# Kernel tuning notes

Hardware: AMD Instinct MI355X
Metric: run time of the kernel (lower is better)

Reference implementation:

```python
import jax, jax.numpy as jnp
import numpy as np

B, S, E, H = 1, 2048, 2048, 16
D = E // H  # head_dim = 128
EPS = 1e-6
NEG_INF = -1e30


def _rms_norm(x, gamma):
    # RMSNorm over last dim: x / sqrt(mean(x^2)+eps) * gamma
    return x * jax.lax.rsqrt(jnp.mean(x * x, axis=-1, keepdims=True) + EPS) * gamma


def _rotate_half(x):
    x1, x2 = jnp.split(x, 2, axis=-1)
    return jnp.concatenate([-x2, x1], axis=-1)


def _rope(x, cos, sin):
    # x: [B,H,S,D]; cos/sin: [S,D] broadcast over batch and heads
    return x * cos + _rotate_half(x) * sin


def setup_inputs() -> dict:
    key = jax.random.key(0)
    ks = jax.random.split(key, 5)
    sc = lambda n: 1.0 / np.sqrt(n)
    x = jax.random.normal(ks[0], (B, S, E), jnp.float32)
    # realistic RoPE tables
    inv_freq = 1.0 / (10000.0 ** (jnp.arange(0, D, 2, dtype=jnp.float32) / D))
    t = jnp.arange(S, dtype=jnp.float32)
    freqs = jnp.outer(t, inv_freq)                    # [S, D/2]
    emb = jnp.concatenate([freqs, freqs], axis=-1)    # [S, D]
    cos, sin = jnp.cos(emb), jnp.sin(emb)
    Wq = jax.random.normal(ks[1], (E, E), jnp.float32) * sc(E)
    Wk = jax.random.normal(ks[2], (D, E), jnp.float32) * sc(E)
    Wv = jax.random.normal(ks[3], (D, E), jnp.float32) * sc(E)
    Wo = jax.random.normal(ks[4], (E, E), jnp.float32) * sc(E)
    q_gamma = jnp.ones((D,), jnp.float32)
    k_gamma = jnp.ones((D,), jnp.float32)
    return dict(x=x, cos=cos, sin=sin, Wq=Wq, Wk=Wk, Wv=Wv, Wo=Wo,
                q_gamma=q_gamma, k_gamma=k_gamma)


def reference(x, cos, sin, Wq, Wk, Wv, Wo, q_gamma, k_gamma):
    # projections (Linear with bias=False -> x @ W.T)
    Q = (x @ Wq.T).reshape(B, S, H, D).transpose(0, 2, 1, 3)  # [B,H,S,D]
    K = (x @ Wk.T)[:, None, :, :]                             # [B,1,S,D]
    V = x @ Wv.T                                              # [B,S,D] (single KV head)
    # qk-norm
    Q = _rms_norm(Q, q_gamma)
    K = _rms_norm(K, k_gamma)  # computed then discarded below (faithful to source)
    # RoPE — source bug replicated: K is overwritten with roped Q
    Q = _rope(Q, cos, sin)
    K = _rope(Q, cos, sin)     # [B,H,S,D]
    # causal attention (dense stand-in for flash_attn_func, scale 1/sqrt(D))
    scores = jnp.einsum('bhqd,bhkd->bhqk', Q, K) / jnp.sqrt(jnp.float32(D))
    causal = jnp.tril(jnp.ones((S, S), bool))
    scores = jnp.where(causal, scores, NEG_INF)
    probs = jax.nn.softmax(scores, axis=-1)
    # single V head broadcast across query heads
    out = jnp.einsum('bhqk,bkd->bqhd', probs, V).reshape(B, S, E)
    return out @ Wo.T
```

## Files before the change

kernel.cpp:

```cpp
#include <hip/hip_runtime.h>
#include <hip/hip_bf16.h>

#define SL 2048
#define NH 16
#define HD 128
#define EMB 2048

typedef __attribute__((ext_vector_type(8))) __bf16 bf16x8;
typedef __attribute__((ext_vector_type(4))) float f32x4;
typedef __attribute__((ext_vector_type(8))) short short8;

__device__ __forceinline__ short bf16bits(float x) {
  union { __hip_bfloat16 h; short s; } u;
  u.h = __float2bfloat16(x);
  return u.s;
}

__device__ __forceinline__ float fexp2(float x) {
  return __builtin_amdgcn_exp2f(x);
}

#define GLDS16(gp, lp) __builtin_amdgcn_global_load_lds( \
    (__attribute__((address_space(1))) void*)(gp), \
    (__attribute__((address_space(3))) void*)(lp), 16, 0, 0)

__global__ __launch_bounds__(256) void cast_all(const float* __restrict__ x,
                                                const float* __restrict__ Wq,
                                                const float* __restrict__ Wv,
                                                const float* __restrict__ Wo,
                                                short* __restrict__ xb,
                                                short* __restrict__ wqvb,
                                                short* __restrict__ wob) {
  long i = ((long)blockIdx.x * 256 + threadIdx.x) * 8;
  const float* in; short* out; long off;
  if (i < 4194304)      { in = x;  out = xb;             off = i; }
  else if (i < 8388608) { in = Wq; out = wqvb;           off = i - 4194304; }
  else if (i < 8650752) { in = Wv; out = wqvb + 4194304; off = i - 8388608; }
  else                  { in = Wo; out = wob;            off = i - 8650752; }
  float4 a = *(const float4*)(in + off);
  float4 b = *(const float4*)(in + off + 4);
  short8 o;
  o[0] = bf16bits(a.x); o[1] = bf16bits(a.y); o[2] = bf16bits(a.z); o[3] = bf16bits(a.w);
  o[4] = bf16bits(b.x); o[5] = bf16bits(b.y); o[6] = bf16bits(b.z); o[7] = bf16bits(b.w);
  *(short8*)(out + off) = o;
}

template<int MODE>
__global__ __launch_bounds__(1024, 1) void gemm128(const short* __restrict__ A,
                                                   const short* __restrict__ B,
                                                   float* __restrict__ C,
                                                   short* __restrict__ Qb,
                                                   short* __restrict__ Kb,
                                                   const float* __restrict__ cosT,
                                                   const float* __restrict__ sinT,
                                                   const float* __restrict__ gamma) {
  __shared__ char arena[131072];
  short* As = (short*)arena;
  const int K = 2048;
  int id = blockIdx.x;
  int nid = (id & 7) * 32 + (id >> 3);
  int tn = nid >> 4, tm = nid & 15;
  int tid = threadIdx.x;
  int w = tid >> 6, lane = tid & 63;
  int g = lane >> 4, c = lane & 15;
  int wr = w >> 2, wc = w & 3;
  const short* Ab = A + (long)(tm * 128) * K;
  const short* Bb = B + (long)(tn * 128) * K;
  int lr = lane >> 3;
  int lsw = (lane & 7) ^ lr;
  int wS = w & 7;
  const short* Sb = (w < 8) ? Ab : Bb;
  int soff = (w < 8) ? 0 : 8192;
  f32x4 zero = {0.f, 0.f, 0.f, 0.f};
  f32x4 acc[2][2];
#pragma unroll
  for (int m = 0; m < 2; ++m)
#pragma unroll
    for (int n = 0; n < 2; ++n) acc[m][n] = zero;

#define STG(buf, kt) do { \
    _Pragma("unroll") \
    for (int j = 0; j < 2; ++j) { \
      int grp = wS * 2 + j; \
      GLDS16(Sb + (long)(grp * 8 + lr) * K + (kt) + lsw * 8, \
             As + (buf) * 16384 + soff + grp * 512); \
    } } while (0)

  STG(0, 0);
  STG(1, 64);
  STG(2, 128);
  asm volatile("s_waitcnt vmcnt(4)" ::: "memory");
  __builtin_amdgcn_s_barrier();

  for (int it = 0; it < 32; ++it) {
    int bf = it & 3;
    if (it < 29) STG((it + 3) & 3, (it + 3) * 64);
    const short* Ax = As + bf * 16384;
    const short* Bx = Ax + 8192;
    bf16x8 af[2][2], bfr[2][2];
#pragma unroll
    for (int kk = 0; kk < 2; ++kk) {
      int ch = ((kk * 4 + g) ^ (c & 7)) * 8;
#pragma unroll
      for (int m = 0; m < 2; ++m)
        af[kk][m] = *(const bf16x8*)(Ax + (wr * 32 + m * 16 + c) * 64 + ch);
#pragma unroll
      for (int n = 0; n < 2; ++n)
        bfr[kk][n] = *(const bf16x8*)(Bx + (wc * 32 + n * 16 + c) * 64 + ch);
    }
    __builtin_amdgcn_s_setprio(1);
#pragma unroll
    for (int kk = 0; kk < 2; ++kk)
#pragma unroll
      for (int m = 0; m < 2; ++m)
#pragma unroll
        for (int n = 0; n < 2; ++n)
          acc[m][n] = __builtin_amdgcn_mfma_f32_16x16x32_bf16(af[kk][m], bfr[kk][n],
                                                              acc[m][n], 0, 0, 0);
    __builtin_amdgcn_s_setprio(0);
    if (it < 29) {
      asm volatile("s_waitcnt vmcnt(4)" ::: "memory");
    } else if (it == 29) {
      asm volatile("s_waitcnt vmcnt(2)" ::: "memory");
    } else if (it == 30) {
      asm volatile("s_waitcnt vmcnt(0)" ::: "memory");
    }
    if (it < 31) __builtin_amdgcn_s_barrier();
  }
#undef STG

  if constexpr (MODE == 0) {
#pragma unroll
    for (int m = 0; m < 2; ++m)
#pragma unroll
      for (int n = 0; n < 2; ++n)
#pragma unroll
        for (int r = 0; r < 4; ++r) {
          int row = tm * 128 + wr * 32 + m * 16 + g * 4 + r;
          int col = tn * 128 + wc * 32 + n * 16 + c;
          C[(long)row * 2048 + col] = acc[m][n][r];
        }
  } else {
    float* xch = (float*)arena;
    float* ssb = (float*)(arena + 65536);
    float ssmr[2][4];
#pragma unroll
    for (int m = 0; m < 2; ++m)
#pragma unroll
      for (int r = 0; r < 4; ++r) {
        float s = acc[m][0][r] * acc[m][0][r] + acc[m][1][r] * acc[m][1][r];
#pragma unroll
        for (int off = 1; off <= 8; off <<= 1) s += __shfl_xor(s, off, 64);
        ssmr[m][r] = s;
      }
    if (c == 0) {
#pragma unroll
      for (int m = 0; m < 2; ++m)
#pragma unroll
        for (int r = 0; r < 4; ++r)
          ssb[wc * 128 + wr * 32 + m * 16 + g * 4 + r] = ssmr[m][r];
    }
#pragma unroll
    for (int m = 0; m < 2; ++m)
#pragma unroll
      for (int n = 0; n < 2; ++n)
#pragma unroll
        for (int r = 0; r < 4; ++r)
          xch[(wr * 32 + m * 16 + g * 4 + r) * 128 + wc * 32 + n * 16 + c] = acc[m][n][r];
    __syncthreads();
    float rn[2][4];
#pragma unroll
    for (int m = 0; m < 2; ++m)
#pragma unroll
      for (int r = 0; r < 4; ++r) {
        int rl = wr * 32 + m * 16 + g * 4 + r;
        float s4 = ssb[rl] + ssb[128 + rl] + ssb[256 + rl] + ssb[384 + rl];
        rn[m][r] = rsqrtf(s4 * (1.0f / 128.0f) + 1e-6f);
      }
    float sgn = (wc < 2) ? -1.f : 1.f;
    float g_own[2], g_par[2];
#pragma unroll
    for (int n = 0; n < 2; ++n) {
      int d = wc * 32 + n * 16 + c;
      g_own[n] = gamma[d];
      g_par[n] = gamma[d ^ 64];
    }
    const float QSC = 0.08838834764831845f * 1.4426950408889634f;
#pragma unroll
    for (int m = 0; m < 2; ++m)
#pragma unroll
      for (int n = 0; n < 2; ++n)
#pragma unroll
        for (int r = 0; r < 4; ++r) {
          int rl = wr * 32 + m * 16 + g * 4 + r;
          int s = tm * 128 + rl;
          int d = wc * 32 + n * 16 + c;
          int u = (wc & 1) * 32 + n * 16 + c;
          float cv = cosT[s * 128 + u];
          float sv = sinT[s * 128 + u];
          float xo = acc[m][n][r] * rn[m][r] * g_own[n];
          float xq = xch[rl * 128 + (d ^ 64)] * rn[m][r] * g_par[n];
          float y  = xo * cv + sgn * xq * sv;
          float yp = xq * cv - sgn * xo * sv;
          float kk = y * cv + sgn * yp * sv;
          long o = ((long)tn * SL + s) * HD + d;
          Qb[o] = bf16bits(y * QSC);
          Kb[o] = bf16bits(kk);
        }
  }
}

__global__ __launch_bounds__(256, 3) void gemm64v(const short* __restrict__ A,
                                                  const short* __restrict__ B,
                                                  short* __restrict__ VT) {
  __shared__ char lds_raw[36864];
  short* As = (short*)lds_raw;
  short* Bs = (short*)(lds_raw + 12288);
  const int K = 2048;
  int nwg = gridDim.x;
  int id = blockIdx.x;
  int nid = (id & 7) * (nwg >> 3) + (id >> 3);
  int tn = 16;
  int tm = nid & 31;
  int tid = threadIdx.x;
  int wave = tid >> 6, lane = tid & 63;
  int g = lane >> 4, c = lane & 15;
  int wr = wave >> 1, wc = wave & 1;
  const short* Ab = A + (long)(tm * 64) * K;
  const short* Bb = B + (long)(tn * 128) * K;
  int swz = (lane & 3) ^ ((lane >> 3) & 3);
  int rdc = (g ^ ((c >> 1) & 3)) * 8;
  f32x4 zero = {0.f, 0.f, 0.f, 0.f};
  f32x4 acc[2][4];
#pragma unroll
  for (int m = 0; m < 2; ++m)
#pragma unroll
    for (int n = 0; n < 4; ++n) acc[m][n] = zero;

#define STG(buf, kt) do { \
    GLDS16(Ab + (long)(wave * 16 + (lane >> 2)) * K + (kt) + swz * 8, \
           As + (buf) * 2048 + wave * 512); \
    _Pragma("unroll") \
    for (int hh = 0; hh < 2; ++hh) { \
      int rb = wave * 32 + hh * 16; \
      GLDS16(Bb + (long)(rb + (lane >> 2)) * K + (kt) + swz * 8, \
             Bs + (buf) * 4096 + rb * 32); \
    } } while (0)

  STG(0, 0);
  STG(1, 32);
  asm volatile("s_waitcnt vmcnt(3)" ::: "memory");
  __builtin_amdgcn_s_barrier();

  int b0 = 0, b1 = 1, b2 = 2;
  for (int it = 0; it < 64; ++it) {
    if (it < 62) STG(b2, (it + 2) * 32);
    bf16x8 a[2], b[4];
#pragma unroll
    for (int m = 0; m < 2; ++m)
      a[m] = *(const bf16x8*)(As + b0 * 2048 + (wr * 32 + m * 16 + c) * 32 + rdc);
#pragma unroll
    for (int n = 0; n < 4; ++n)
      b[n] = *(const bf16x8*)(Bs + b0 * 4096 + (wc * 64 + n * 16 + c) * 32 + rdc);
    __builtin_amdgcn_s_setprio(1);
#pragma unroll
    for (int m = 0; m < 2; ++m)
#pragma unroll
      for (int n = 0; n < 4; ++n)
        acc[m][n] = __builtin_amdgcn_mfma_f32_16x16x32_bf16(a[m], b[n], acc[m][n], 0, 0, 0);
    __builtin_amdgcn_s_setprio(0);
    if (it < 62) {
      asm volatile("s_waitcnt vmcnt(3)" ::: "memory");
      __builtin_amdgcn_s_barrier();
    } else if (it == 62) {
      asm volatile("s_waitcnt vmcnt(0)" ::: "memory");
      __builtin_amdgcn_s_barrier();
    }
    int t = b0; b0 = b1; b1 = b2; b2 = t;
  }
#undef STG

#pragma unroll
  for (int m = 0; m < 2; ++m)
#pragma unroll
    for (int n = 0; n < 4; ++n)
#pragma unroll
      for (int r = 0; r < 4; ++r) {
        int s = tm * 64 + wr * 32 + m * 16 + g * 4 + r;
        int d = wc * 64 + n * 16 + c;
        VT[(long)d * SL + s] = bf16bits(acc[m][n][r]);
      }
}

__global__ __launch_bounds__(256, 2) void attn_part(const short* __restrict__ Qb,
                                                    const short* __restrict__ Kb,
                                                    const short* __restrict__ VTg,
                                                    short* __restrict__ att,
                                                    float* __restrict__ pO,
                                                    float* __restrict__ pml) {
  __shared__ short Ks[2][64 * 128];
  __shared__ short Vs[2][128 * 64];
  __shared__ short Ps[4][16 * 72];
  int wave = threadIdx.x >> 6, lane = threadIdx.x & 63;
  int g = lane >> 4, c = lane & 15;
  int id = blockIdx.x;
  int h = ((id & 7) << 1) | (id >> 8);
  int x = (id >> 3) & 15;
  int cbk = (id >> 7) & 1;
  const short* Qh = Qb + (long)h * SL * HD;
  const short* Kh = Kb + (long)h * SL * HD;
  f32x4 zero = {0.f, 0.f, 0.f, 0.f};
  const float THR2 = 11.541560327111707f;

  int pqt[2], plo[2], pcnt[2], pout[2];
  if (cbk == 0) {
    pqt[0] = x;      plo[0] = 0;      pcnt[0] = x + 1;  pout[0] = 0;
    pqt[1] = 31 - x; plo[1] = 0;      pcnt[1] = 16 - x; pout[1] = 1;
  } else {
    pqt[0] = 31 - x; plo[0] = 16 - x; pcnt[0] = 16;     pout[0] = 2;
    pqt[1] = 0;      plo[1] = 0;      pcnt[1] = 0;      pout[1] = 0;
  }
  int total = pcnt[0] + pcnt[1];

#define ASTAGE(b, kvb) do { \
    _Pragma("unroll") \
    for (int i = 0; i < 4; ++i) { \
      int rb = wave * 16 + i * 4; \
      int row = rb + (lane >> 4); \
      int c16 = (lane & 15) ^ (row & 7); \
      GLDS16(Kh + (long)((kvb) + row) * HD + c16 * 8, &Ks[b][rb * 128]); \
    } \
    _Pragma("unroll") \
    for (int i = 0; i < 4; ++i) { \
      int dbase = i * 32 + wave * 8; \
      int drow = dbase + (lane >> 3); \
      int u8 = (lane & 7) ^ (drow & 7); \
      GLDS16(VTg + (long)drow * SL + (kvb) + u8 * 8, &Vs[b][dbase * 64]); \
    } } while (0)

  ASTAGE(0, plo[0] * 64);
  int s = 0;

  for (int p = 0; p < 2; ++p) {
    int nt = pcnt[p];
    if (nt == 0) break;
    int qt = pqt[p];
    int qb = qt * 64 + wave * 16;
    int qown = qb + c;

    bf16x8 aq[4];
#pragma unroll
    for (int kc = 0; kc < 4; ++kc)
      aq[kc] = *(const bf16x8*)(Qh + (long)qown * HD + kc * 32 + g * 8);

    float m = -1e30f, l = 0.f;
    f32x4 O[8];
#pragma unroll
    for (int d8 = 0; d8 < 8; ++d8) O[d8] = zero;

    for (int i = 0; i < nt; ++i, ++s) {
      int kt = plo[p] + i;
      int kvb = kt * 64;
      int bcu = s & 1;
      asm volatile("s_waitcnt vmcnt(0)" ::: "memory");
      __builtin_amdgcn_s_barrier();
      {
        int ns = s + 1;
        if (ns < total) {
          int np = (ns < pcnt[0]) ? 0 : 1;
          int nkt = plo[np] + (ns - (np ? pcnt[0] : 0));
          ASTAGE(bcu ^ 1, nkt * 64);
        }
      }

      f32x4 sf[4];
#pragma unroll
      for (int n = 0; n < 4; ++n) sf[n] = zero;
      __builtin_amdgcn_s_setprio(1);
#pragma unroll
      for (int kc = 0; kc < 4; ++kc)
#pragma unroll
        for (int n = 0; n < 4; ++n) {
          int row = n * 16 + c;
          int u = (kc * 4 + g) ^ (row & 7);
          bf16x8 bk = *(const bf16x8*)(&Ks[bcu][row * 128 + u * 8]);
          sf[n] = __builtin_amdgcn_mfma_f32_16x16x32_bf16(bk, aq[kc], sf[n], 0, 0, 0);
        }
      __builtin_amdgcn_s_setprio(0);

      float pm = -1e30f;
      if (kt == qt) {
#pragma unroll
        for (int n = 0; n < 4; ++n) {
#pragma unroll
          for (int r = 0; r < 4; ++r) {
            int k = kvb + n * 16 + g * 4 + r;
            if (k > qown) sf[n][r] = -1e30f;
          }
          float a0 = fmaxf(sf[n][0], sf[n][1]);
          float a1 = fmaxf(sf[n][2], sf[n][3]);
          pm = fmaxf(pm, fmaxf(a0, a1));
        }
      } else {
#pragma unroll
        for (int n = 0; n < 4; ++n) {
          float a0 = fmaxf(sf[n][0], sf[n][1]);
          float a1 = fmaxf(sf[n][2], sf[n][3]);
          pm = fmaxf(pm, fmaxf(a0, a1));
        }
      }
      pm = fmaxf(pm, __shfl_xor(pm, 16, 64));
      pm = fmaxf(pm, __shfl_xor(pm, 32, 64));

      if (__any(pm > m + THR2)) {
        float mn_ = fmaxf(m, pm);
        float corr = fexp2(m - mn_);
        m = mn_;
        l *= corr;
        float c4[4];
#pragma unroll
        for (int r = 0; r < 4; ++r) c4[r] = __shfl(corr, g * 4 + r, 64);
#pragma unroll
        for (int d8 = 0; d8 < 8; ++d8)
#pragma unroll
          for (int r = 0; r < 4; ++r) O[d8][r] *= c4[r];
      }

#pragma unroll
      for (int n = 0; n < 4; ++n) {
        float p0 = fexp2(sf[n][0] - m);
        float p1 = fexp2(sf[n][1] - m);
        float p2 = fexp2(sf[n][2] - m);
        float p3 = fexp2(sf[n][3] - m);
        l += (p0 + p1) + (p2 + p3);
        unsigned lo = (unsigned)(unsigned short)bf16bits(p0) |
                      ((unsigned)(unsigned short)bf16bits(p1) << 16);
        unsigned hi = (unsigned)(unsigned short)bf16bits(p2) |
                      ((unsigned)(unsigned short)bf16bits(p3) << 16);
        unsigned long long pq = (unsigned long long)lo | ((unsigned long long)hi << 32);
        *(unsigned long long*)&Ps[wave][c * 72 + n * 16 + g * 4] = pq;
      }

#pragma unroll
      for (int k2 = 0; k2 < 2; ++k2) {
        bf16x8 ap = *(const bf16x8*)(&Ps[wave][c * 72 + k2 * 32 + g * 8]);
        __builtin_amdgcn_s_setprio(1);
#pragma unroll
        for (int d8 = 0; d8 < 8; ++d8) {
          int drow = d8 * 16 + c;
          int u = (k2 * 4 + g) ^ (c & 7);
          bf16x8 bv = *(const bf16x8*)(&Vs[bcu][drow * 64 + u * 8]);
          O[d8] = __builtin_amdgcn_mfma_f32_16x16x32_bf16(ap, bv, O[d8], 0, 0, 0);
        }
        __builtin_amdgcn_s_setprio(0);
      }
    }

    if (pout[p] == 0) {
      float lf = l;
      lf += __shfl_xor(lf, 16, 64);
      lf += __shfl_xor(lf, 32, 64);
      float rinv = 1.0f / lf;
      float r4[4];
#pragma unroll
      for (int r = 0; r < 4; ++r) r4[r] = __shfl(rinv, g * 4 + r, 64);
#pragma unroll
      for (int d8 = 0; d8 < 8; ++d8)
#pragma unroll
        for (int r = 0; r < 4; ++r) {
          int q = qb + g * 4 + r;
          att[(long)q * EMB + h * HD + d8 * 16 + c] = bf16bits(O[d8][r] * r4[r]);
        }
    } else {
      int part = pout[p] - 1;
      float lf = l;
      lf += __shfl_xor(lf, 16, 64);
      lf += __shfl_xor(lf, 32, 64);
      float* Op = pO + ((long)(part * 16 + x) * 16 + h) * 8192;
#pragma unroll
      for (int d8 = 0; d8 < 8; ++d8)
#pragma unroll
        for (int r = 0; r < 4; ++r)
          Op[(wave * 16 + g * 4 + r) * 128 + d8 * 16 + c] = O[d8][r];
      if (g == 0) {
        float* pmb = pml + ((part * 16 + x) * 16 + h) * 64 + wave * 16 + c;
        pmb[0]     = m;
        pmb[32768] = lf;
      }
    }
  }
#undef ASTAGE
}

__global__ __launch_bounds__(256) void attn_comb(const float* __restrict__ pO,
                                                 const float* __restrict__ pml,
                                                 short* __restrict__ att) {
  int b = blockIdx.x;
  int x = b & 15, h = b >> 4;
  int qt = 31 - x;
  int t = threadIdx.x;
  int q = t >> 2, d0 = (t & 3) * 32;
  int i0 = (x * 16 + h) * 64 + q;
  int i1 = (256 + x * 16 + h) * 64 + q;
  float m0 = pml[i0], m1 = pml[i1];
  float l0 = pml[32768 + i0], l1 = pml[32768 + i1];
  float M = fmaxf(m0, m1);
  float w0 = __builtin_amdgcn_exp2f(m0 - M), w1 = __builtin_amdgcn_exp2f(m1 - M);
  float inv = 1.0f / (l0 * w0 + l1 * w1);
  const float* O0 = pO + ((long)(x * 16 + h)) * 8192 + q * 128 + d0;
  const float* O1 = pO + ((long)(256 + x * 16 + h)) * 8192 + q * 128 + d0;
  short* out = att + (long)(qt * 64 + q) * EMB + h * HD + d0;
#pragma unroll
  for (int j = 0; j < 32; j += 4) {
    float4 a = *(const float4*)(O0 + j);
    float4 bb = *(const float4*)(O1 + j);
    out[j + 0] = bf16bits((a.x * w0 + bb.x * w1) * inv);
    out[j + 1] = bf16bits((a.y * w0 + bb.y * w1) * inv);
    out[j + 2] = bf16bits((a.z * w0 + bb.z * w1) * inv);
    out[j + 3] = bf16bits((a.w * w0 + bb.w * w1) * inv);
  }
}

extern "C" void kernel_launch(void* const* d_in, const int* in_sizes, int n_in,
                              void* d_out, int out_size, void* d_ws, size_t ws_size,
                              hipStream_t stream) {
  const float* x    = (const float*)d_in[0];
  const float* cosT = (const float*)d_in[1];
  const float* sinT = (const float*)d_in[2];
  const float* Wq   = (const float*)d_in[3];
  const float* Wv   = (const float*)d_in[5];
  const float* Wo   = (const float*)d_in[6];
  const float* qg   = (const float*)d_in[7];

  char* w = (char*)d_ws;
  short* xb   = (short*)(w + 0);
  short* wqvb = (short*)(w + 8388608);
  short* wob  = (short*)(w + 17301504);
  short* vt   = (short*)(w + 25690112);
  short* qb   = (short*)(w + 26214400);
  short* kb   = (short*)(w + 34603008);
  short* attb = (short*)(w + 42991616);
  float* pO   = (float*)(w + 0);
  float* pml  = (float*)(w + 16777216);

  cast_all<<<dim3(6272), dim3(256), 0, stream>>>(x, Wq, Wv, Wo, xb, wqvb, wob);

  gemm128<1><<<dim3(256), dim3(1024), 0, stream>>>(xb, wqvb, nullptr, qb, kb,
                                                   cosT, sinT, qg);
  gemm64v<<<dim3(32), dim3(256), 0, stream>>>(xb, wqvb, vt);
  attn_part<<<dim3(512), dim3(256), 0, stream>>>(qb, kb, vt, attb, pO, pml);
  attn_comb<<<dim3(256), dim3(256), 0, stream>>>(pO, pml, attb);
  gemm128<0><<<dim3(256), dim3(1024), 0, stream>>>(attb, wob, (float*)d_out,
                                                   nullptr, nullptr,
                                                   nullptr, nullptr, nullptr);
}
```

Baseline: 125.7 us.

## Pre-swizzle weights into MFMA fragment layout and load B operand directly to registers

The cast kernel now writes Wq and Wo in a chunked column-major layout that matches the MFMA B-fragment order. The 128x128 GEMM stops staging B through LDS and loads B fragments straight from global memory into registers, double-buffered across two k-steps. Only A still goes through the LDS pipeline. This halves LDS traffic and staging instructions per iteration, but moves B reads onto global/L2 with no reuse across waves sharing columns, and it reshuffles the workspace offsets.

```diff
diff --git a/kernel.cpp b/kernel.cpp
--- a/kernel.cpp
+++ b/kernel.cpp
@@ -29,33 +29,40 @@
                                                 const float* __restrict__ Wv,
                                                 const float* __restrict__ Wo,
                                                 short* __restrict__ xb,
-                                                short* __restrict__ wqvb,
-                                                short* __restrict__ wob) {
+                                                short* __restrict__ wqc,
+                                                short* __restrict__ wvb,
+                                                short* __restrict__ woc) {
   long i = ((long)blockIdx.x * 256 + threadIdx.x) * 8;
-  const float* in; short* out; long off;
-  if (i < 4194304)      { in = x;  out = xb;             off = i; }
-  else if (i < 8388608) { in = Wq; out = wqvb;           off = i - 4194304; }
-  else if (i < 8650752) { in = Wv; out = wqvb + 4194304; off = i - 8388608; }
-  else                  { in = Wo; out = wob;            off = i - 8650752; }
+  const float* in; short* out; long off; int ck = 0;
+  if (i < 4194304)      { in = x;  out = xb;  off = i; }
+  else if (i < 8388608) { in = Wq; out = wqc; off = i - 4194304; ck = 1; }
+  else if (i < 8650752) { in = Wv; out = wvb; off = i - 8388608; }
+  else                  { in = Wo; out = woc; off = i - 8650752; ck = 1; }
   float4 a = *(const float4*)(in + off);
   float4 b = *(const float4*)(in + off + 4);
   short8 o;
   o[0] = bf16bits(a.x); o[1] = bf16bits(a.y); o[2] = bf16bits(a.z); o[3] = bf16bits(a.w);
   o[4] = bf16bits(b.x); o[5] = bf16bits(b.y); o[6] = bf16bits(b.z); o[7] = bf16bits(b.w);
-  *(short8*)(out + off) = o;
+  long dst = off;
+  if (ck) {
+    long col = off >> 11, k0 = off & 2047;
+    dst = ((k0 >> 3) * 2048 + col) * 8;
+  }
+  *(short8*)(out + dst) = o;
 }
 
 template<int MODE>
 __global__ __launch_bounds__(1024, 1) void gemm128(const short* __restrict__ A,
-                                                   const short* __restrict__ B,
+                                                   const short* __restrict__ Bc,
                                                    float* __restrict__ C,
                                                    short* __restrict__ Qb,
                                                    short* __restrict__ Kb,
                                                    const float* __restrict__ cosT,
                                                    const float* __restrict__ sinT,
                                                    const float* __restrict__ gamma) {
-  __shared__ char arena[131072];
-  short* As = (short*)arena;
+  __shared__ short As[4 * 8192];
+  __shared__ float xch[16384];
+  __shared__ float ssb[512];
   const int K = 2048;
   int id = blockIdx.x;
   int nid = (id & 7) * 32 + (id >> 3);
@@ -65,12 +72,9 @@
   int g = lane >> 4, c = lane & 15;
   int wr = w >> 2, wc = w & 3;
   const short* Ab = A + (long)(tm * 128) * K;
-  const short* Bb = B + (long)(tn * 128) * K;
   int lr = lane >> 3;
   int lsw = (lane & 7) ^ lr;
-  int wS = w & 7;
-  const short* Sb = (w < 8) ? Ab : Bb;
-  int soff = (w < 8) ? 0 : 8192;
+  int bcol = tn * 128 + wc * 32 + c;
   f32x4 zero = {0.f, 0.f, 0.f, 0.f};
   f32x4 acc[2][2];
 #pragma unroll
@@ -78,56 +82,67 @@
 #pragma unroll
     for (int n = 0; n < 2; ++n) acc[m][n] = zero;
 
-#define STG(buf, kt) do { \
+#define STG(buf, kt) GLDS16(Ab + (long)(w * 8 + lr) * K + (kt) + lsw * 8, \
+                            As + (buf) * 8192 + w * 512)
+#define LOADB(dst, t) do { \
+    int chb = (t) * 8; \
     _Pragma("unroll") \
-    for (int j = 0; j < 2; ++j) { \
-      int grp = wS * 2 + j; \
-      GLDS16(Sb + (long)(grp * 8 + lr) * K + (kt) + lsw * 8, \
-             As + (buf) * 16384 + soff + grp * 512); \
-    } } while (0)
-
+    for (int kk2 = 0; kk2 < 2; ++kk2) \
+      _Pragma("unroll") \
+      for (int n2 = 0; n2 < 2; ++n2) \
+        dst[kk2][n2] = *(const bf16x8*)(Bc + \
+            ((long)(chb + kk2 * 4 + g) * 2048 + bcol + n2 * 16) * 8); \
+    } while (0)
+#define COMP(t, bfr) do { \
+    const short* Ax = As + ((t) & 3) * 8192; \
+    bf16x8 af[2][2]; \
+    _Pragma("unroll") \
+    for (int kk2 = 0; kk2 < 2; ++kk2) { \
+      int ch = ((kk2 * 4 + g) ^ (c & 7)) * 8; \
+      _Pragma("unroll") \
+      for (int m2 = 0; m2 < 2; ++m2) \
+        af[kk2][m2] = *(const bf16x8*)(Ax + (wr * 32 + m2 * 16 + c) * 64 + ch); \
+    } \
+    __builtin_amdgcn_s_setprio(1); \
+    _Pragma("unroll") \
+    for (int kk2 = 0; kk2 < 2; ++kk2) \
+      _Pragma("unroll") \
+      for (int m2 = 0; m2 < 2; ++m2) \
+        _Pragma("unroll") \
+        for (int n2 = 0; n2 < 2; ++n2) \
+          acc[m2][n2] = __builtin_amdgcn_mfma_f32_16x16x32_bf16(af[kk2][m2], \
+                            bfr[kk2][n2], acc[m2][n2], 0, 0, 0); \
+    __builtin_amdgcn_s_setprio(0); \
+  } while (0)
+
+  bf16x8 bfrA[2][2], bfrB[2][2];
   STG(0, 0);
   STG(1, 64);
   STG(2, 128);
-  asm volatile("s_waitcnt vmcnt(4)" ::: "memory");
+  LOADB(bfrA, 0);
+  asm volatile("s_waitcnt vmcnt(6)" ::: "memory");
   __builtin_amdgcn_s_barrier();
 
-  for (int it = 0; it < 32; ++it) {
-    int bf = it & 3;
-    if (it < 29) STG((it + 3) & 3, (it + 3) * 64);
-    const short* Ax = As + bf * 16384;
-    const short* Bx = Ax + 8192;
-    bf16x8 af[2][2], bfr[2][2];
-#pragma unroll
-    for (int kk = 0; kk < 2; ++kk) {
-      int ch = ((kk * 4 + g) ^ (c & 7)) * 8;
-#pragma unroll
-      for (int m = 0; m < 2; ++m)
-        af[kk][m] = *(const bf16x8*)(Ax + (wr * 32 + m * 16 + c) * 64 + ch);
-#pragma unroll
-      for (int n = 0; n < 2; ++n)
-        bfr[kk][n] = *(const bf16x8*)(Bx + (wc * 32 + n * 16 + c) * 64 + ch);
+  for (int bt = 0; bt < 16; ++bt) {
+    int t0 = bt * 2, t1 = t0 + 1;
+    if (t0 <= 28) STG((t0 + 3) & 3, (t0 + 3) * 64);
+    LOADB(bfrB, t0 + 1);
+    COMP(t0, bfrA);
+    if (t0 <= 28) asm volatile("s_waitcnt vmcnt(6)" ::: "memory");
+    else          asm volatile("s_waitcnt vmcnt(4)" ::: "memory");
+    __builtin_amdgcn_s_barrier();
+    if (t1 <= 28) STG((t1 + 3) & 3, (t1 + 3) * 64);
+    if (t1 < 31) LOADB(bfrA, t1 + 1);
+    COMP(t1, bfrB);
+    if (t1 < 31) {
+      if (t1 <= 28) asm volatile("s_waitcnt vmcnt(6)" ::: "memory");
+      else          asm volatile("s_waitcnt vmcnt(4)" ::: "memory");
+      __builtin_amdgcn_s_barrier();
     }
-    __builtin_amdgcn_s_setprio(1);
-#pragma unroll
-    for (int kk = 0; kk < 2; ++kk)
-#pragma unroll
-      for (int m = 0; m < 2; ++m)
-#pragma unroll
-        for (int n = 0; n < 2; ++n)
-          acc[m][n] = __builtin_amdgcn_mfma_f32_16x16x32_bf16(af[kk][m], bfr[kk][n],
-                                                              acc[m][n], 0, 0, 0);
-    __builtin_amdgcn_s_setprio(0);
-    if (it < 29) {
-      asm volatile("s_waitcnt vmcnt(4)" ::: "memory");
-    } else if (it == 29) {
-      asm volatile("s_waitcnt vmcnt(2)" ::: "memory");
-    } else if (it == 30) {
-      asm volatile("s_waitcnt vmcnt(0)" ::: "memory");
-    }
-    if (it < 31) __builtin_amdgcn_s_barrier();
   }
 #undef STG
+#undef LOADB
+#undef COMP
 
   if constexpr (MODE == 0) {
 #pragma unroll
@@ -141,8 +156,6 @@
           C[(long)row * 2048 + col] = acc[m][n][r];
         }
   } else {
-    float* xch = (float*)arena;
-    float* ssb = (float*)(arena + 65536);
     float ssmr[2][4];
 #pragma unroll
     for (int m = 0; m < 2; ++m)
@@ -220,14 +233,13 @@
   int nwg = gridDim.x;
   int id = blockIdx.x;
   int nid = (id & 7) * (nwg >> 3) + (id >> 3);
-  int tn = 16;
   int tm = nid & 31;
   int tid = threadIdx.x;
   int wave = tid >> 6, lane = tid & 63;
   int g = lane >> 4, c = lane & 15;
   int wr = wave >> 1, wc = wave & 1;
   const short* Ab = A + (long)(tm * 64) * K;
-  const short* Bb = B + (long)(tn * 128) * K;
+  const short* Bb = B;
   int swz = (lane & 3) ^ ((lane >> 3) & 3);
   int rdc = (g ^ ((c >> 1) & 3)) * 8;
   f32x4 zero = {0.f, 0.f, 0.f, 0.f};
@@ -534,23 +546,24 @@
 
   char* w = (char*)d_ws;
   short* xb   = (short*)(w + 0);
-  short* wqvb = (short*)(w + 8388608);
-  short* wob  = (short*)(w + 17301504);
+  short* wqc  = (short*)(w + 8388608);
+  short* woc  = (short*)(w + 16777216);
+  short* wvb  = (short*)(w + 25165824);
   short* vt   = (short*)(w + 25690112);
   short* qb   = (short*)(w + 26214400);
   short* kb   = (short*)(w + 34603008);
   short* attb = (short*)(w + 42991616);
   float* pO   = (float*)(w + 0);
-  float* pml  = (float*)(w + 16777216);
-
-  cast_all<<<dim3(6272), dim3(256), 0, stream>>>(x, Wq, Wv, Wo, xb, wqvb, wob);
-
-  gemm128<1><<<dim3(256), dim3(1024), 0, stream>>>(xb, wqvb, nullptr, qb, kb,
+  float* pml  = (float*)(w + 51380224);
+
+  cast_all<<<dim3(6272), dim3(256), 0, stream>>>(x, Wq, Wv, Wo, xb, wqc, wvb, woc);
+
+  gemm128<1><<<dim3(256), dim3(1024), 0, stream>>>(xb, wqc, nullptr, qb, kb,
                                                    cosT, sinT, qg);
-  gemm64v<<<dim3(32), dim3(256), 0, stream>>>(xb, wqvb, vt);
+  gemm64v<<<dim3(32), dim3(256), 0, stream>>>(xb, wvb, vt);
   attn_part<<<dim3(512), dim3(256), 0, stream>>>(qb, kb, vt, attb, pO, pml);
   attn_comb<<<dim3(256), dim3(256), 0, stream>>>(pO, pml, attb);
-  gemm128<0><<<dim3(256), dim3(1024), 0, stream>>>(attb, wob, (float*)d_out,
+  gemm128<0><<<dim3(256), dim3(1024), 0, stream>>>(attb, woc, (float*)d_out,
                                                    nullptr, nullptr,
                                                    nullptr, nullptr, nullptr);
 }
```

Measured after the change: 154.1 us. +22.6%, slower.

## Split-K the V projection GEMM across 256 workgroups with a reduction kernel

Applied to the files above, without the earlier changes.

The V projection GEMM previously ran on only 32 workgroups, each iterating the full K=2048, which leaves most CUs idle. It now splits K into 8 chunks of 256, giving 256 workgroups that each write fp32 partial sums to a workspace buffer. A new combine kernel sums the 8 partials, transposes the result through LDS and writes bf16 V^T. This adds an extra launch and about 8 MB of fp32 partial traffic, and it reuses the attention-output workspace region for the partials.

```diff
diff --git a/kernel.cpp b/kernel.cpp
--- a/kernel.cpp
+++ b/kernel.cpp
@@ -210,24 +210,24 @@
   }
 }
 
-__global__ __launch_bounds__(256, 3) void gemm64v(const short* __restrict__ A,
-                                                  const short* __restrict__ B,
-                                                  short* __restrict__ VT) {
+__global__ __launch_bounds__(256, 3) void gemm64v_sk(const short* __restrict__ A,
+                                                     const short* __restrict__ B,
+                                                     float* __restrict__ pv) {
   __shared__ char lds_raw[36864];
   short* As = (short*)lds_raw;
   short* Bs = (short*)(lds_raw + 12288);
   const int K = 2048;
-  int nwg = gridDim.x;
   int id = blockIdx.x;
-  int nid = (id & 7) * (nwg >> 3) + (id >> 3);
-  int tn = 16;
+  int nid = (id & 7) * 32 + (id >> 3);
+  int kc = nid >> 5;
   int tm = nid & 31;
+  int k0 = kc * 256;
   int tid = threadIdx.x;
   int wave = tid >> 6, lane = tid & 63;
   int g = lane >> 4, c = lane & 15;
   int wr = wave >> 1, wc = wave & 1;
   const short* Ab = A + (long)(tm * 64) * K;
-  const short* Bb = B + (long)(tn * 128) * K;
+  const short* Bb = B + (long)(16 * 128) * K;
   int swz = (lane & 3) ^ ((lane >> 3) & 3);
   int rdc = (g ^ ((c >> 1) & 3)) * 8;
   f32x4 zero = {0.f, 0.f, 0.f, 0.f};
@@ -247,14 +247,14 @@
              Bs + (buf) * 4096 + rb * 32); \
     } } while (0)
 
-  STG(0, 0);
-  STG(1, 32);
+  STG(0, k0);
+  STG(1, k0 + 32);
   asm volatile("s_waitcnt vmcnt(3)" ::: "memory");
   __builtin_amdgcn_s_barrier();
 
   int b0 = 0, b1 = 1, b2 = 2;
-  for (int it = 0; it < 64; ++it) {
-    if (it < 62) STG(b2, (it + 2) * 32);
+  for (int it = 0; it < 8; ++it) {
+    if (it < 6) STG(b2, k0 + (it + 2) * 32);
     bf16x8 a[2], b[4];
 #pragma unroll
     for (int m = 0; m < 2; ++m)
@@ -269,10 +269,10 @@
       for (int n = 0; n < 4; ++n)
         acc[m][n] = __builtin_amdgcn_mfma_f32_16x16x32_bf16(a[m], b[n], acc[m][n], 0, 0, 0);
     __builtin_amdgcn_s_setprio(0);
-    if (it < 62) {
+    if (it < 6) {
       asm volatile("s_waitcnt vmcnt(3)" ::: "memory");
       __builtin_amdgcn_s_barrier();
-    } else if (it == 62) {
+    } else if (it == 6) {
       asm volatile("s_waitcnt vmcnt(0)" ::: "memory");
       __builtin_amdgcn_s_barrier();
     }
@@ -288,8 +288,32 @@
       for (int r = 0; r < 4; ++r) {
         int s = tm * 64 + wr * 32 + m * 16 + g * 4 + r;
         int d = wc * 64 + n * 16 + c;
-        VT[(long)d * SL + s] = bf16bits(acc[m][n][r]);
-      }
+        pv[(long)kc * 262144 + (long)s * 128 + d] = acc[m][n][r];
+      }
+}
+
+__global__ __launch_bounds__(256) void comb64v(const float* __restrict__ pv,
+                                               short* __restrict__ VT) {
+  __shared__ float ttile[8][128];
+  int b = blockIdx.x;
+  int t = threadIdx.x;
+  int d = t & 127, sh = t >> 7;
+#pragma unroll
+  for (int j = 0; j < 4; ++j) {
+    int s = b * 8 + sh * 4 + j;
+    float sum = 0.f;
+#pragma unroll
+    for (int kc = 0; kc < 8; ++kc)
+      sum += pv[(long)kc * 262144 + (long)s * 128 + d];
+    ttile[sh * 4 + j][d] = sum;
+  }
+  __syncthreads();
+  if (t < 128) {
+    short8 o;
+#pragma unroll
+    for (int j = 0; j < 8; ++j) o[j] = bf16bits(ttile[j][t]);
+    *(short8*)(VT + (long)t * SL + b * 8) = o;
+  }
 }
 
 __global__ __launch_bounds__(256, 2) void attn_part(const short* __restrict__ Qb,
@@ -540,6 +564,7 @@
   short* qb   = (short*)(w + 26214400);
   short* kb   = (short*)(w + 34603008);
   short* attb = (short*)(w + 42991616);
+  float* pv   = (float*)(w + 42991616);
   float* pO   = (float*)(w + 0);
   float* pml  = (float*)(w + 16777216);
 
@@ -547,7 +572,8 @@
 
   gemm128<1><<<dim3(256), dim3(1024), 0, stream>>>(xb, wqvb, nullptr, qb, kb,
                                                    cosT, sinT, qg);
-  gemm64v<<<dim3(32), dim3(256), 0, stream>>>(xb, wqvb, vt);
+  gemm64v_sk<<<dim3(256), dim3(256), 0, stream>>>(xb, wqvb, pv);
+  comb64v<<<dim3(256), dim3(256), 0, stream>>>(pv, vt);
   attn_part<<<dim3(512), dim3(256), 0, stream>>>(qb, kb, vt, attb, pO, pml);
   attn_comb<<<dim3(256), dim3(256), 0, stream>>>(pO, pml, attb);
   gemm128<0><<<dim3(256), dim3(1024), 0, stream>>>(attb, wob, (float*)d_out,
```

After: 117.1 us. 1.07x faster.
